# Optimization experiments

Measured on AMD Instinct MI355X. Metric: run time of the kernel, lower is better.

Reference implementation:

```python
import jax, jax.numpy as jnp
import numpy as np

N_HEAD = 16
MASK_VALUE = -10000.0


def setup_inputs() -> dict:
    key = jax.random.key(0)
    k1, k2, k3 = jax.random.split(key, 3)
    B, S, D = 2, 2048, 1024
    x = jax.random.normal(k1, (B, S, D), dtype=jnp.float32)
    W_qkv = jax.random.normal(k2, (D, 3 * D), dtype=jnp.float32) * 0.02
    b_qkv = jnp.zeros((3 * D,), dtype=jnp.float32)
    W_out = jax.random.normal(k3, (D, D), dtype=jnp.float32) * 0.02
    b_out = jnp.zeros((D,), dtype=jnp.float32)
    return {"x": x, "W_qkv": W_qkv, "b_qkv": b_qkv, "W_out": W_out, "b_out": b_out}


def reference(x, W_qkv, b_qkv, W_out, b_out):
    B, S, D = x.shape
    H = N_HEAD
    hd = D // H
    # fused QKV projection
    qkv = x @ W_qkv + b_qkv                      # [B, S, 3D]
    q, k, v = jnp.split(qkv, 3, axis=-1)
    # split heads -> [B, H, S, hd]
    def split_heads(t):
        return t.reshape(B, S, H, hd).transpose(0, 2, 1, 3)
    q, k, v = split_heads(q), split_heads(k), split_heads(v)
    # scaled causal attention with explicit mask-fill (matches ops.attention)
    scale = 1.0 / jnp.sqrt(jnp.asarray(hd, dtype=x.dtype))
    w = jnp.einsum('bhqd,bhkd->bhqk', q, k) * scale   # [B, H, S, S]
    causal = jnp.tril(jnp.ones((S, S), dtype=bool))    # [S, S]
    w = jnp.where(causal, w, jnp.asarray(MASK_VALUE, dtype=w.dtype))
    a = jax.nn.softmax(w, axis=-1)
    o = jnp.einsum('bhqk,bhkd->bhqd', a, v)            # [B, H, S, hd]
    # merge heads -> [B, S, D]
    o = o.transpose(0, 2, 1, 3).reshape(B, S, D)
    out = o @ W_out + b_out
    return out
```

## Files before the change

kernel.cpp:

```cpp
#include <hip/hip_runtime.h>
#include <hip/hip_bf16.h>
#include <stdint.h>

#define BATCH 2
#define SEQ   2048
#define DIM   1024
#define NH    16
#define HD    64
#define MVAL  (-10000.0f)

#if __has_builtin(__builtin_amdgcn_exp2f)
#define EXP2(x) __builtin_amdgcn_exp2f(x)
#define QSCALE  (0.125f * 1.44269504f)
#else
#define EXP2(x) __expf(x)
#define QSCALE  0.125f
#endif

typedef __attribute__((ext_vector_type(8))) short bf16x8;
typedef __attribute__((ext_vector_type(4))) float f32x4;
typedef unsigned short u16;

static __device__ __forceinline__ u16 f2bf(float f) {
  union { float f; uint32_t u; } c; c.f = f;
  uint32_t x = c.u;
  return (u16)((x + 0x7fffu + ((x >> 16) & 1u)) >> 16);
}

static __device__ __forceinline__ uint32_t pk2(float a, float b) {
  __hip_bfloat162 h = __float22bfloat162_rn(make_float2(a, b));
  union { __hip_bfloat162 h; uint32_t u; } c; c.h = h;
  return c.u;
}

static __device__ __forceinline__ int swz128(int row, int chunk) {
  return row * 128 + (((chunk ^ (row & 7)) & 7) << 4);
}

static __device__ __forceinline__ void gload_lds16(const void* g, void* l) {
  __builtin_amdgcn_global_load_lds((const __attribute__((address_space(1))) void*)g,
                                   (__attribute__((address_space(3))) void*)l, 16, 0, 0);
}

__global__ void prep_kernel(const float* __restrict__ x, u16* __restrict__ xb,
                            const float* __restrict__ Wqkv, u16* __restrict__ WqkvT,
                            const float* __restrict__ Wout, u16* __restrict__ WoutT) {
  __shared__ float tile[32][33];
  int blk = blockIdx.x, tid = threadIdx.x;
  if (blk < 4096) {
    int i = blk * 256 + tid;
    float4 v = reinterpret_cast<const float4*>(x)[i];
    reinterpret_cast<uint2*>(xb)[i] = make_uint2(pk2(v.x, v.y), pk2(v.z, v.w));
    return;
  }
  const float* in;
  u16* out;
  int C, t;
  if (blk < 4096 + 3072) { t = blk - 4096; in = Wqkv; out = WqkvT; C = 3072; }
  else                   { t = blk - 7168; in = Wout; out = WoutT; C = 1024; }
  int R = DIM;
  int c0 = (t % (C / 32)) * 32, r0 = (t / (C / 32)) * 32;
  int tx = tid & 31, ty = tid >> 5;
#pragma unroll
  for (int i = 0; i < 32; i += 8)
    tile[ty + i][tx] = in[(size_t)(r0 + ty + i) * C + c0 + tx];
  __syncthreads();
#pragma unroll
  for (int i = 0; i < 32; i += 8)
    out[(size_t)(c0 + ty + i) * R + r0 + tx] = f2bf(tile[tx][ty + i]);
}

template <int EPI>
__global__ __launch_bounds__(256, 2) void gemm_bt_kernel(
    const u16* __restrict__ A, const u16* __restrict__ Bt,
    const float* __restrict__ bias, float* __restrict__ Cout,
    u16* __restrict__ Qo, u16* __restrict__ Ko, u16* __restrict__ Vto,
    int M, int N, int K) {
  __shared__ __align__(16) char lds[32768];
  char* As = lds;
  char* Bs = lds + 16384;
  int tid = threadIdx.x;
  int lane = tid & 63, l15 = lane & 15, l4 = lane >> 4;
  int w = tid >> 6, wr = w >> 1, wc = w & 1;
  int m0 = blockIdx.y * 128, n0 = blockIdx.x * 128;
  int srow = tid >> 3, sch = tid & 7;
  int sc_swz = ((sch ^ (srow & 7)) << 3);

  const u16* Ap = A + (size_t)(m0 + srow) * K + sc_swz;
  const u16* Bp = Bt + (size_t)(n0 + srow) * K + sc_swz;

  f32x4 acc[4][4] = {};

  for (int k0 = 0; k0 < K; k0 += 64) {
    __syncthreads();
#pragma unroll
    for (int i = 0; i < 4; i++) {
      gload_lds16(Ap + (size_t)i * 32 * K + k0, As + i * 4096 + tid * 16);
      gload_lds16(Bp + (size_t)i * 32 * K + k0, Bs + i * 4096 + tid * 16);
    }
    __syncthreads();
#pragma unroll
    for (int ks = 0; ks < 2; ks++) {
      int ch = ks * 4 + l4;
      bf16x8 af[4], bfv[4];
#pragma unroll
      for (int mi = 0; mi < 4; mi++)
        af[mi] = *reinterpret_cast<const bf16x8*>(As + swz128(wr * 64 + mi * 16 + l15, ch));
#pragma unroll
      for (int nj = 0; nj < 4; nj++)
        bfv[nj] = *reinterpret_cast<const bf16x8*>(Bs + swz128(wc * 64 + nj * 16 + l15, ch));
#pragma unroll
      for (int nj = 0; nj < 4; nj++)
#pragma unroll
        for (int mi = 0; mi < 4; mi++)
          acc[nj][mi] = __builtin_amdgcn_mfma_f32_16x16x32_bf16(bfv[nj], af[mi], acc[nj][mi], 0, 0, 0);
    }
  }

#pragma unroll
  for (int nj = 0; nj < 4; nj++) {
    int nb = n0 + wc * 64 + nj * 16 + l4 * 4;
    float4 bv = *reinterpret_cast<const float4*>(bias + nb);
#pragma unroll
    for (int mi = 0; mi < 4; mi++) {
      int m = m0 + wr * 64 + mi * 16 + l15;
      f32x4 a = acc[nj][mi];
      float v0 = a[0] + bv.x, v1 = a[1] + bv.y, v2 = a[2] + bv.z, v3 = a[3] + bv.w;
      if (EPI == 1) {
        *reinterpret_cast<float4*>(Cout + (size_t)m * N + nb) = make_float4(v0, v1, v2, v3);
      } else {
        int b = m >> 11, s = m & 2047;
        int sec = nb >> 10, c = nb & 1023, h = c >> 6, d = c & 63;
        size_t bh = (size_t)(b * NH + h);
        if (sec == 0) {
          *reinterpret_cast<uint2*>(Qo + (bh * SEQ + s) * HD + d) =
              make_uint2(pk2(v0 * QSCALE, v1 * QSCALE), pk2(v2 * QSCALE, v3 * QSCALE));
        } else if (sec == 1) {
          *reinterpret_cast<uint2*>(Ko + (bh * SEQ + s) * HD + d) =
              make_uint2(pk2(v0, v1), pk2(v2, v3));
        } else {
          u16* vt = Vto + (bh * HD + d) * SEQ + s;
          vt[0]       = f2bf(v0);
          vt[SEQ]     = f2bf(v1);
          vt[2 * SEQ] = f2bf(v2);
          vt[3 * SEQ] = f2bf(v3);
        }
      }
    }
  }
}

__global__ __launch_bounds__(256, 2) void attn_kernel(
    const u16* __restrict__ Q, const u16* __restrict__ K,
    const u16* __restrict__ Vt, u16* __restrict__ O) {
  __shared__ __align__(16) char lds[81920];
  int tid = threadIdx.x, lane = tid & 63, w = tid >> 6;
  int l15 = lane & 15, l4 = lane >> 4;
  int sub = w & 1, par = w >> 1;
  int blk = blockIdx.x;
  int bh = (blk & 7) * 4 + ((blk >> 3) & 3);
  int p = blk >> 5;
  const u16* Qh = Q + (size_t)bh * SEQ * HD;
  const u16* Kh = K + (size_t)bh * SEQ * HD;
  const u16* Vh = Vt + (size_t)bh * HD * SEQ;
  char* Pw = lds + 65536 + w * 4096;
  int srow = tid >> 3, sch = tid & 7;
  int b_ = bh >> 4, h_ = bh & 15;

  bf16x8 onesf;
#pragma unroll
  for (int j = 0; j < 8; j++) onesf[j] = (short)0x3F80;

  auto stageKV = [&](int b, int T) {
    const u16* Kt = Kh + (size_t)T * 128 * HD;
    const u16* Vs = Vh + (size_t)T * 128;
    char* Kb = lds + b * 16384;
    char* Vb = lds + 32768 + b * 16384;
#pragma unroll
    for (int i = 0; i < 4; i++) {
      int row = i * 32 + srow;
      int c = (sch ^ (row & 7)) << 3;
      gload_lds16(Kt + (size_t)row * HD + c, Kb + row * 128 + sch * 16);
    }
#pragma unroll
    for (int sv = 0; sv < 2; sv++)
#pragma unroll
      for (int i = 0; i < 2; i++) {
        int d = i * 32 + srow;
        int c = (sch ^ (d & 7)) << 3;
        gload_lds16(Vs + (size_t)d * SEQ + sv * 64 + c, Vb + sv * 8192 + d * 128 + sch * 16);
      }
  };

  int buf = 0;
  stageKV(0, 0);
  __syncthreads();

  for (int pass = 0; pass < 2; pass++) {
    int qt = (pass == 0) ? (31 - p) : p;
    int nT = (qt + 2) >> 1;
    int qb = qt * 64 + sub * 32;

    bf16x8 qf[2][2];
#pragma unroll
    for (int mi = 0; mi < 2; mi++)
#pragma unroll
      for (int ks = 0; ks < 2; ks++)
        qf[mi][ks] = *reinterpret_cast<const bf16x8*>(
            Qh + (size_t)(qb + mi * 16 + l15) * HD + ks * 32 + l4 * 8);

    float mrun[2] = {-1e30f, -1e30f};
    f32x4 oacc[4][2] = {};
    f32x4 acc_l[2] = {};
    bf16x8 pf_c[2][2], vf_c[4][2];
    bool pend = false;

    for (int T = 0; T < nT; T++) {
      int nxt = (T + 1 < nT) ? (T + 1) : (pass == 0 ? 0 : -1);
      if (nxt >= 0) stageKV(buf ^ 1, nxt);

      char* Kw = lds + buf * 16384 + par * 8192;
      char* Vw = lds + 32768 + buf * 16384 + par * 8192;
      int kvb = T * 128 + par * 64;

      __builtin_amdgcn_s_setprio(1);
      if (pend) {
#pragma unroll
        for (int ks = 0; ks < 2; ks++) {
#pragma unroll
          for (int nd = 0; nd < 4; nd++)
#pragma unroll
            for (int mi = 0; mi < 2; mi++)
              oacc[nd][mi] = __builtin_amdgcn_mfma_f32_16x16x32_bf16(
                  vf_c[nd][ks], pf_c[mi][ks], oacc[nd][mi], 0, 0, 0);
#pragma unroll
          for (int mi = 0; mi < 2; mi++)
            acc_l[mi] = __builtin_amdgcn_mfma_f32_16x16x32_bf16(
                onesf, pf_c[mi][ks], acc_l[mi], 0, 0, 0);
        }
      }

      f32x4 s[4][2] = {};
#pragma unroll
      for (int ks = 0; ks < 2; ks++)
#pragma unroll
        for (int nj = 0; nj < 4; nj++) {
          bf16x8 kf = *reinterpret_cast<const bf16x8*>(Kw + swz128(nj * 16 + l15, ks * 4 + l4));
#pragma unroll
          for (int mi = 0; mi < 2; mi++)
            s[nj][mi] = __builtin_amdgcn_mfma_f32_16x16x32_bf16(kf, qf[mi][ks], s[nj][mi], 0, 0, 0);
        }
      __builtin_amdgcn_s_setprio(0);

#pragma unroll
      for (int ks = 0; ks < 2; ks++)
#pragma unroll
        for (int nd = 0; nd < 4; nd++)
          vf_c[nd][ks] = *reinterpret_cast<const bf16x8*>(Vw + swz128(nd * 16 + l15, ks * 4 + l4));

      if (kvb + 63 > qb) {
#pragma unroll
        for (int nj = 0; nj < 4; nj++)
#pragma unroll
          for (int mi = 0; mi < 2; mi++) {
            int qg = qb + mi * 16 + l15;
#pragma unroll
            for (int r = 0; r < 4; r++) {
              int kg = kvb + nj * 16 + l4 * 4 + r;
              if (kg > qg) s[nj][mi][r] = MVAL;
            }
          }
      }

      float mt[2];
#pragma unroll
      for (int mi = 0; mi < 2; mi++) {
        float m = s[0][mi][0];
#pragma unroll
        for (int nj = 0; nj < 4; nj++)
#pragma unroll
          for (int r = 0; r < 4; r++) m = fmaxf(m, s[nj][mi][r]);
        m = fmaxf(m, __shfl_xor(m, 16));
        m = fmaxf(m, __shfl_xor(m, 32));
        mt[mi] = m;
      }

      if (!__all((mt[0] <= mrun[0]) & (mt[1] <= mrun[1]))) {
#pragma unroll
        for (int mi = 0; mi < 2; mi++) {
          float mnew = fmaxf(mrun[mi], mt[mi]);
          float alpha = EXP2(mrun[mi] - mnew);
          mrun[mi] = mnew;
#pragma unroll
          for (int nd = 0; nd < 4; nd++)
#pragma unroll
            for (int r = 0; r < 4; r++) oacc[nd][mi][r] *= alpha;
#pragma unroll
          for (int r = 0; r < 4; r++) acc_l[mi][r] *= alpha;
        }
      }

#pragma unroll
      for (int mi = 0; mi < 2; mi++) {
        int prow = mi * 16 + l15;
#pragma unroll
        for (int nj = 0; nj < 4; nj++) {
          float p0 = EXP2(s[nj][mi][0] - mrun[mi]);
          float p1 = EXP2(s[nj][mi][1] - mrun[mi]);
          float p2 = EXP2(s[nj][mi][2] - mrun[mi]);
          float p3 = EXP2(s[nj][mi][3] - mrun[mi]);
          int chunk = nj * 2 + (l4 >> 1);
          char* dst = Pw + prow * 128 + (((chunk ^ (prow & 7)) & 7) << 4) + (l4 & 1) * 8;
          *reinterpret_cast<uint2*>(dst) = make_uint2(pk2(p0, p1), pk2(p2, p3));
        }
      }

      asm volatile("s_waitcnt lgkmcnt(0)" ::: "memory");
      __builtin_amdgcn_sched_barrier(0);

#pragma unroll
      for (int mi = 0; mi < 2; mi++)
#pragma unroll
        for (int ks = 0; ks < 2; ks++)
          pf_c[mi][ks] = *reinterpret_cast<const bf16x8*>(Pw + swz128(mi * 16 + l15, ks * 4 + l4));
      pend = true;

      __syncthreads();
      buf ^= 1;
    }

    __builtin_amdgcn_s_setprio(1);
#pragma unroll
    for (int ks = 0; ks < 2; ks++) {
#pragma unroll
      for (int nd = 0; nd < 4; nd++)
#pragma unroll
        for (int mi = 0; mi < 2; mi++)
          oacc[nd][mi] = __builtin_amdgcn_mfma_f32_16x16x32_bf16(
              vf_c[nd][ks], pf_c[mi][ks], oacc[nd][mi], 0, 0, 0);
#pragma unroll
      for (int mi = 0; mi < 2; mi++)
        acc_l[mi] = __builtin_amdgcn_mfma_f32_16x16x32_bf16(
            onesf, pf_c[mi][ks], acc_l[mi], 0, 0, 0);
    }
    __builtin_amdgcn_s_setprio(0);

    char* Xo = lds + (buf ^ 1) * 16384;
    float* Xml = (float*)(lds + 65536);
    if (par == 1) {
#pragma unroll
      for (int mi = 0; mi < 2; mi++) {
        int row = sub * 32 + mi * 16 + l15;
        if (l4 == 0) {
          Xml[row * 2] = mrun[mi];
          Xml[row * 2 + 1] = acc_l[mi][0];
        }
#pragma unroll
        for (int nd = 0; nd < 4; nd++)
          *reinterpret_cast<f32x4*>(Xo + row * 256 + (((nd * 4 + l4) ^ (row & 7)) << 4)) =
              oacc[nd][mi];
      }
    }
    __syncthreads();
    if (par == 0) {
#pragma unroll
      for (int mi = 0; mi < 2; mi++) {
        int row = sub * 32 + mi * 16 + l15;
        float mB = Xml[row * 2], lB = Xml[row * 2 + 1];
        float m = fmaxf(mrun[mi], mB);
        float wA = EXP2(mrun[mi] - m), wB = EXP2(mB - m);
        float linv = 1.0f / (acc_l[mi][0] * wA + lB * wB);
        float fA = wA * linv, fB = wB * linv;
        u16* orow = O + ((size_t)b_ * SEQ + qt * 64 + sub * 32 + mi * 16 + l15) * DIM + h_ * HD;
#pragma unroll
        for (int nd = 0; nd < 4; nd++) {
          f32x4 ob = *reinterpret_cast<const f32x4*>(
              Xo + row * 256 + (((nd * 4 + l4) ^ (row & 7)) << 4));
          float o0 = oacc[nd][mi][0] * fA + ob[0] * fB;
          float o1 = oacc[nd][mi][1] * fA + ob[1] * fB;
          float o2 = oacc[nd][mi][2] * fA + ob[2] * fB;
          float o3 = oacc[nd][mi][3] * fA + ob[3] * fB;
          *reinterpret_cast<uint2*>(orow + nd * 16 + l4 * 4) = make_uint2(pk2(o0, o1), pk2(o2, o3));
        }
      }
    }
    __syncthreads();
  }
}

extern "C" void kernel_launch(void* const* d_in, const int* in_sizes, int n_in,
                              void* d_out, int out_size, void* d_ws, size_t ws_size,
                              hipStream_t stream) {
  const float* x     = (const float*)d_in[0];
  const float* W_qkv = (const float*)d_in[1];
  const float* b_qkv = (const float*)d_in[2];
  const float* W_out = (const float*)d_in[3];
  const float* b_out = (const float*)d_in[4];
  float* out = (float*)d_out;
  char* ws = (char*)d_ws;

  u16* xb    = (u16*)(ws);
  u16* WqkvT = (u16*)(ws + 8388608);
  u16* WoutT = (u16*)(ws + 8388608 + 6291456);
  u16* Qb    = (u16*)(ws + 16777216);
  u16* Kb    = (u16*)(ws + 16777216 + 8388608);
  u16* Vtb   = (u16*)(ws + 16777216 + 2 * 8388608);
  u16* Ob    = (u16*)(ws + 16777216 + 3 * 8388608);

  prep_kernel<<<4096 + 3072 + 1024, 256, 0, stream>>>(x, xb, W_qkv, WqkvT, W_out, WoutT);
  gemm_bt_kernel<0><<<dim3(3 * DIM / 128, BATCH * SEQ / 128), 256, 0, stream>>>(
      xb, WqkvT, b_qkv, nullptr, Qb, Kb, Vtb, BATCH * SEQ, 3 * DIM, DIM);
  attn_kernel<<<512, 256, 0, stream>>>(Qb, Kb, Vtb, Ob);
  gemm_bt_kernel<1><<<dim3(DIM / 128, BATCH * SEQ / 128), 256, 0, stream>>>(
      Ob, WoutT, b_out, out, nullptr, nullptr, nullptr, BATCH * SEQ, DIM, DIM);
}
```

Measured before the change: 112.0 us.

## Process both paired query tiles in one KV sweep sharing K/V loads

Instead of two sequential passes over KV for the long (31-p) and short (p) query tiles, the kernel now runs a single KV loop and computes both tiles' scores and outputs from the same staged K/V blocks. This halves K/V global staging for the overlapping range and removes the second pass's pipeline ramp and the extra epilogue barrier. The cost is doubled accumulator register state (two sets of oacc, mrun and acc_l), which raises register pressure against the two-blocks-per-CU launch bound. The previous software pipelining of the PV MFMA into the next iteration is also dropped, and both tiles' P matrices now share the same per-wave LDS scratch in turn.

```diff
diff --git a/kernel.cpp b/kernel.cpp
--- a/kernel.cpp
+++ b/kernel.cpp
@@ -160,6 +160,9 @@
   int blk = blockIdx.x;
   int bh = (blk & 7) * 4 + ((blk >> 3) & 3);
   int p = blk >> 5;
+  int qtA = 31 - p, qtB = p;
+  int nTA = (qtA + 2) >> 1, nTB = (qtB + 2) >> 1;
+  int qbA = qtA * 64 + sub * 32, qbB = qtB * 64 + sub * 32;
   const u16* Qh = Q + (size_t)bh * SEQ * HD;
   const u16* Kh = K + (size_t)bh * SEQ * HD;
   const u16* Vh = Vt + (size_t)bh * HD * SEQ;
@@ -192,86 +195,64 @@
       }
   };
 
+  bf16x8 qfA[2][2], qfB[2][2];
+#pragma unroll
+  for (int mi = 0; mi < 2; mi++)
+#pragma unroll
+    for (int ks = 0; ks < 2; ks++) {
+      qfA[mi][ks] = *reinterpret_cast<const bf16x8*>(
+          Qh + (size_t)(qbA + mi * 16 + l15) * HD + ks * 32 + l4 * 8);
+      qfB[mi][ks] = *reinterpret_cast<const bf16x8*>(
+          Qh + (size_t)(qbB + mi * 16 + l15) * HD + ks * 32 + l4 * 8);
+    }
+
+  float mrunA[2] = {-1e30f, -1e30f}, mrunB[2] = {-1e30f, -1e30f};
+  f32x4 oaccA[4][2] = {}, oaccB[4][2] = {};
+  f32x4 acclA[2] = {}, acclB[2] = {};
+
   int buf = 0;
   stageKV(0, 0);
   __syncthreads();
 
-  for (int pass = 0; pass < 2; pass++) {
-    int qt = (pass == 0) ? (31 - p) : p;
-    int nT = (qt + 2) >> 1;
-    int qb = qt * 64 + sub * 32;
-
-    bf16x8 qf[2][2];
-#pragma unroll
-    for (int mi = 0; mi < 2; mi++)
-#pragma unroll
-      for (int ks = 0; ks < 2; ks++)
-        qf[mi][ks] = *reinterpret_cast<const bf16x8*>(
-            Qh + (size_t)(qb + mi * 16 + l15) * HD + ks * 32 + l4 * 8);
-
-    float mrun[2] = {-1e30f, -1e30f};
-    f32x4 oacc[4][2] = {};
-    f32x4 acc_l[2] = {};
-    bf16x8 pf_c[2][2], vf_c[4][2];
-    bool pend = false;
-
-    for (int T = 0; T < nT; T++) {
-      int nxt = (T + 1 < nT) ? (T + 1) : (pass == 0 ? 0 : -1);
-      if (nxt >= 0) stageKV(buf ^ 1, nxt);
-
-      char* Kw = lds + buf * 16384 + par * 8192;
-      char* Vw = lds + 32768 + buf * 16384 + par * 8192;
-      int kvb = T * 128 + par * 64;
-
-      __builtin_amdgcn_s_setprio(1);
-      if (pend) {
-#pragma unroll
-        for (int ks = 0; ks < 2; ks++) {
-#pragma unroll
-          for (int nd = 0; nd < 4; nd++)
-#pragma unroll
-            for (int mi = 0; mi < 2; mi++)
-              oacc[nd][mi] = __builtin_amdgcn_mfma_f32_16x16x32_bf16(
-                  vf_c[nd][ks], pf_c[mi][ks], oacc[nd][mi], 0, 0, 0);
-#pragma unroll
-          for (int mi = 0; mi < 2; mi++)
-            acc_l[mi] = __builtin_amdgcn_mfma_f32_16x16x32_bf16(
-                onesf, pf_c[mi][ks], acc_l[mi], 0, 0, 0);
-        }
-      }
-
-      f32x4 s[4][2] = {};
-#pragma unroll
-      for (int ks = 0; ks < 2; ks++)
-#pragma unroll
-        for (int nj = 0; nj < 4; nj++) {
-          bf16x8 kf = *reinterpret_cast<const bf16x8*>(Kw + swz128(nj * 16 + l15, ks * 4 + l4));
-#pragma unroll
-          for (int mi = 0; mi < 2; mi++)
-            s[nj][mi] = __builtin_amdgcn_mfma_f32_16x16x32_bf16(kf, qf[mi][ks], s[nj][mi], 0, 0, 0);
-        }
-      __builtin_amdgcn_s_setprio(0);
-
-#pragma unroll
-      for (int ks = 0; ks < 2; ks++)
-#pragma unroll
-        for (int nd = 0; nd < 4; nd++)
-          vf_c[nd][ks] = *reinterpret_cast<const bf16x8*>(Vw + swz128(nd * 16 + l15, ks * 4 + l4));
-
-      if (kvb + 63 > qb) {
-#pragma unroll
-        for (int nj = 0; nj < 4; nj++)
-#pragma unroll
-          for (int mi = 0; mi < 2; mi++) {
-            int qg = qb + mi * 16 + l15;
-#pragma unroll
-            for (int r = 0; r < 4; r++) {
-              int kg = kvb + nj * 16 + l4 * 4 + r;
-              if (kg > qg) s[nj][mi][r] = MVAL;
-            }
+  for (int T = 0; T < nTA; T++) {
+    if (T + 1 < nTA) stageKV(buf ^ 1, T + 1);
+    char* Kw = lds + buf * 16384 + par * 8192;
+    char* Vw = lds + 32768 + buf * 16384 + par * 8192;
+    int kvb = T * 128 + par * 64;
+    bool doB = (T < nTB);
+
+    bf16x8 kf[2][4];
+#pragma unroll
+    for (int ks = 0; ks < 2; ks++)
+#pragma unroll
+      for (int nj = 0; nj < 4; nj++)
+        kf[ks][nj] = *reinterpret_cast<const bf16x8*>(Kw + swz128(nj * 16 + l15, ks * 4 + l4));
+
+    f32x4 s[4][2] = {};
+    __builtin_amdgcn_s_setprio(1);
+#pragma unroll
+    for (int ks = 0; ks < 2; ks++)
+#pragma unroll
+      for (int nj = 0; nj < 4; nj++)
+#pragma unroll
+        for (int mi = 0; mi < 2; mi++)
+          s[nj][mi] = __builtin_amdgcn_mfma_f32_16x16x32_bf16(kf[ks][nj], qfA[mi][ks], s[nj][mi], 0, 0, 0);
+    __builtin_amdgcn_s_setprio(0);
+
+    if (kvb + 63 > qbA) {
+#pragma unroll
+      for (int nj = 0; nj < 4; nj++)
+#pragma unroll
+        for (int mi = 0; mi < 2; mi++) {
+          int qg = qbA + mi * 16 + l15;
+#pragma unroll
+          for (int r = 0; r < 4; r++) {
+            int kg = kvb + nj * 16 + l4 * 4 + r;
+            if (kg > qg) s[nj][mi][r] = MVAL;
           }
-      }
-
+        }
+    }
+    {
       float mt[2];
 #pragma unroll
       for (int mi = 0; mi < 2; mi++) {
@@ -284,107 +265,230 @@
         m = fmaxf(m, __shfl_xor(m, 32));
         mt[mi] = m;
       }
-
-      if (!__all((mt[0] <= mrun[0]) & (mt[1] <= mrun[1]))) {
+      if (!__all((mt[0] <= mrunA[0]) & (mt[1] <= mrunA[1]))) {
 #pragma unroll
         for (int mi = 0; mi < 2; mi++) {
-          float mnew = fmaxf(mrun[mi], mt[mi]);
-          float alpha = EXP2(mrun[mi] - mnew);
-          mrun[mi] = mnew;
+          float mnew = fmaxf(mrunA[mi], mt[mi]);
+          float alpha = EXP2(mrunA[mi] - mnew);
+          mrunA[mi] = mnew;
 #pragma unroll
           for (int nd = 0; nd < 4; nd++)
 #pragma unroll
-            for (int r = 0; r < 4; r++) oacc[nd][mi][r] *= alpha;
-#pragma unroll
-          for (int r = 0; r < 4; r++) acc_l[mi][r] *= alpha;
-        }
-      }
-
+            for (int r = 0; r < 4; r++) oaccA[nd][mi][r] *= alpha;
+#pragma unroll
+          for (int r = 0; r < 4; r++) acclA[mi][r] *= alpha;
+        }
+      }
 #pragma unroll
       for (int mi = 0; mi < 2; mi++) {
         int prow = mi * 16 + l15;
 #pragma unroll
         for (int nj = 0; nj < 4; nj++) {
-          float p0 = EXP2(s[nj][mi][0] - mrun[mi]);
-          float p1 = EXP2(s[nj][mi][1] - mrun[mi]);
-          float p2 = EXP2(s[nj][mi][2] - mrun[mi]);
-          float p3 = EXP2(s[nj][mi][3] - mrun[mi]);
+          float p0 = EXP2(s[nj][mi][0] - mrunA[mi]);
+          float p1 = EXP2(s[nj][mi][1] - mrunA[mi]);
+          float p2 = EXP2(s[nj][mi][2] - mrunA[mi]);
+          float p3 = EXP2(s[nj][mi][3] - mrunA[mi]);
           int chunk = nj * 2 + (l4 >> 1);
           char* dst = Pw + prow * 128 + (((chunk ^ (prow & 7)) & 7) << 4) + (l4 & 1) * 8;
           *reinterpret_cast<uint2*>(dst) = make_uint2(pk2(p0, p1), pk2(p2, p3));
         }
       }
-
+    }
+
+    f32x4 sB[4][2] = {};
+    if (doB) {
+      __builtin_amdgcn_s_setprio(1);
+#pragma unroll
+      for (int ks = 0; ks < 2; ks++)
+#pragma unroll
+        for (int nj = 0; nj < 4; nj++)
+#pragma unroll
+          for (int mi = 0; mi < 2; mi++)
+            sB[nj][mi] = __builtin_amdgcn_mfma_f32_16x16x32_bf16(kf[ks][nj], qfB[mi][ks], sB[nj][mi], 0, 0, 0);
+      __builtin_amdgcn_s_setprio(0);
+    }
+
+    asm volatile("s_waitcnt lgkmcnt(0)" ::: "memory");
+    __builtin_amdgcn_sched_barrier(0);
+    bf16x8 pfA[2][2];
+#pragma unroll
+    for (int mi = 0; mi < 2; mi++)
+#pragma unroll
+      for (int ks = 0; ks < 2; ks++)
+        pfA[mi][ks] = *reinterpret_cast<const bf16x8*>(Pw + swz128(mi * 16 + l15, ks * 4 + l4));
+
+    if (doB) {
+      if (kvb + 63 > qbB) {
+#pragma unroll
+        for (int nj = 0; nj < 4; nj++)
+#pragma unroll
+          for (int mi = 0; mi < 2; mi++) {
+            int qg = qbB + mi * 16 + l15;
+#pragma unroll
+            for (int r = 0; r < 4; r++) {
+              int kg = kvb + nj * 16 + l4 * 4 + r;
+              if (kg > qg) sB[nj][mi][r] = MVAL;
+            }
+          }
+      }
+      float mt[2];
+#pragma unroll
+      for (int mi = 0; mi < 2; mi++) {
+        float m = sB[0][mi][0];
+#pragma unroll
+        for (int nj = 0; nj < 4; nj++)
+#pragma unroll
+          for (int r = 0; r < 4; r++) m = fmaxf(m, sB[nj][mi][r]);
+        m = fmaxf(m, __shfl_xor(m, 16));
+        m = fmaxf(m, __shfl_xor(m, 32));
+        mt[mi] = m;
+      }
+      if (!__all((mt[0] <= mrunB[0]) & (mt[1] <= mrunB[1]))) {
+#pragma unroll
+        for (int mi = 0; mi < 2; mi++) {
+          float mnew = fmaxf(mrunB[mi], mt[mi]);
+          float alpha = EXP2(mrunB[mi] - mnew);
+          mrunB[mi] = mnew;
+#pragma unroll
+          for (int nd = 0; nd < 4; nd++)
+#pragma unroll
+            for (int r = 0; r < 4; r++) oaccB[nd][mi][r] *= alpha;
+#pragma unroll
+          for (int r = 0; r < 4; r++) acclB[mi][r] *= alpha;
+        }
+      }
+#pragma unroll
+      for (int mi = 0; mi < 2; mi++) {
+        int prow = mi * 16 + l15;
+#pragma unroll
+        for (int nj = 0; nj < 4; nj++) {
+          float p0 = EXP2(sB[nj][mi][0] - mrunB[mi]);
+          float p1 = EXP2(sB[nj][mi][1] - mrunB[mi]);
+          float p2 = EXP2(sB[nj][mi][2] - mrunB[mi]);
+          float p3 = EXP2(sB[nj][mi][3] - mrunB[mi]);
+          int chunk = nj * 2 + (l4 >> 1);
+          char* dst = Pw + prow * 128 + (((chunk ^ (prow & 7)) & 7) << 4) + (l4 & 1) * 8;
+          *reinterpret_cast<uint2*>(dst) = make_uint2(pk2(p0, p1), pk2(p2, p3));
+        }
+      }
+    }
+
+    bf16x8 vf[4][2];
+#pragma unroll
+    for (int ks = 0; ks < 2; ks++)
+#pragma unroll
+      for (int nd = 0; nd < 4; nd++)
+        vf[nd][ks] = *reinterpret_cast<const bf16x8*>(Vw + swz128(nd * 16 + l15, ks * 4 + l4));
+
+    __builtin_amdgcn_s_setprio(1);
+#pragma unroll
+    for (int ks = 0; ks < 2; ks++) {
+#pragma unroll
+      for (int nd = 0; nd < 4; nd++)
+#pragma unroll
+        for (int mi = 0; mi < 2; mi++)
+          oaccA[nd][mi] = __builtin_amdgcn_mfma_f32_16x16x32_bf16(
+              vf[nd][ks], pfA[mi][ks], oaccA[nd][mi], 0, 0, 0);
+#pragma unroll
+      for (int mi = 0; mi < 2; mi++)
+        acclA[mi] = __builtin_amdgcn_mfma_f32_16x16x32_bf16(onesf, pfA[mi][ks], acclA[mi], 0, 0, 0);
+    }
+    __builtin_amdgcn_s_setprio(0);
+
+    if (doB) {
       asm volatile("s_waitcnt lgkmcnt(0)" ::: "memory");
       __builtin_amdgcn_sched_barrier(0);
-
+      bf16x8 pfB[2][2];
 #pragma unroll
       for (int mi = 0; mi < 2; mi++)
 #pragma unroll
         for (int ks = 0; ks < 2; ks++)
-          pf_c[mi][ks] = *reinterpret_cast<const bf16x8*>(Pw + swz128(mi * 16 + l15, ks * 4 + l4));
-      pend = true;
-
-      __syncthreads();
-      buf ^= 1;
-    }
-
-    __builtin_amdgcn_s_setprio(1);
-#pragma unroll
-    for (int ks = 0; ks < 2; ks++) {
-#pragma unroll
-      for (int nd = 0; nd < 4; nd++)
+          pfB[mi][ks] = *reinterpret_cast<const bf16x8*>(Pw + swz128(mi * 16 + l15, ks * 4 + l4));
+      __builtin_amdgcn_s_setprio(1);
+#pragma unroll
+      for (int ks = 0; ks < 2; ks++) {
+#pragma unroll
+        for (int nd = 0; nd < 4; nd++)
+#pragma unroll
+          for (int mi = 0; mi < 2; mi++)
+            oaccB[nd][mi] = __builtin_amdgcn_mfma_f32_16x16x32_bf16(
+                vf[nd][ks], pfB[mi][ks], oaccB[nd][mi], 0, 0, 0);
 #pragma unroll
         for (int mi = 0; mi < 2; mi++)
-          oacc[nd][mi] = __builtin_amdgcn_mfma_f32_16x16x32_bf16(
-              vf_c[nd][ks], pf_c[mi][ks], oacc[nd][mi], 0, 0, 0);
-#pragma unroll
-      for (int mi = 0; mi < 2; mi++)
-        acc_l[mi] = __builtin_amdgcn_mfma_f32_16x16x32_bf16(
-            onesf, pf_c[mi][ks], acc_l[mi], 0, 0, 0);
-    }
-    __builtin_amdgcn_s_setprio(0);
-
-    char* Xo = lds + (buf ^ 1) * 16384;
-    float* Xml = (float*)(lds + 65536);
-    if (par == 1) {
-#pragma unroll
-      for (int mi = 0; mi < 2; mi++) {
-        int row = sub * 32 + mi * 16 + l15;
-        if (l4 == 0) {
-          Xml[row * 2] = mrun[mi];
-          Xml[row * 2 + 1] = acc_l[mi][0];
-        }
-#pragma unroll
-        for (int nd = 0; nd < 4; nd++)
-          *reinterpret_cast<f32x4*>(Xo + row * 256 + (((nd * 4 + l4) ^ (row & 7)) << 4)) =
-              oacc[nd][mi];
-      }
-    }
+          acclB[mi] = __builtin_amdgcn_mfma_f32_16x16x32_bf16(onesf, pfB[mi][ks], acclB[mi], 0, 0, 0);
+      }
+      __builtin_amdgcn_s_setprio(0);
+    }
+
     __syncthreads();
-    if (par == 0) {
-#pragma unroll
-      for (int mi = 0; mi < 2; mi++) {
-        int row = sub * 32 + mi * 16 + l15;
-        float mB = Xml[row * 2], lB = Xml[row * 2 + 1];
-        float m = fmaxf(mrun[mi], mB);
-        float wA = EXP2(mrun[mi] - m), wB = EXP2(mB - m);
-        float linv = 1.0f / (acc_l[mi][0] * wA + lB * wB);
+    buf ^= 1;
+  }
+
+  char* XoA = lds + buf * 16384;
+  char* XoB = lds + 32768 + buf * 16384;
+  float* XmlA = (float*)(lds + 65536);
+  float* XmlB = (float*)(lds + 65536 + 8192);
+  if (par == 1) {
+#pragma unroll
+    for (int mi = 0; mi < 2; mi++) {
+      int row = sub * 32 + mi * 16 + l15;
+      if (l4 == 0) {
+        XmlA[row * 2] = mrunA[mi];
+        XmlA[row * 2 + 1] = acclA[mi][0];
+        XmlB[row * 2] = mrunB[mi];
+        XmlB[row * 2 + 1] = acclB[mi][0];
+      }
+#pragma unroll
+      for (int nd = 0; nd < 4; nd++) {
+        *reinterpret_cast<f32x4*>(XoA + row * 256 + (((nd * 4 + l4) ^ (row & 7)) << 4)) =
+            oaccA[nd][mi];
+        *reinterpret_cast<f32x4*>(XoB + row * 256 + (((nd * 4 + l4) ^ (row & 7)) << 4)) =
+            oaccB[nd][mi];
+      }
+    }
+  }
+  __syncthreads();
+  if (par == 0) {
+#pragma unroll
+    for (int mi = 0; mi < 2; mi++) {
+      int row = sub * 32 + mi * 16 + l15;
+      {
+        float mB = XmlA[row * 2], lB = XmlA[row * 2 + 1];
+        float m = fmaxf(mrunA[mi], mB);
+        float wA = EXP2(mrunA[mi] - m), wB = EXP2(mB - m);
+        float linv = 1.0f / (acclA[mi][0] * wA + lB * wB);
         float fA = wA * linv, fB = wB * linv;
-        u16* orow = O + ((size_t)b_ * SEQ + qt * 64 + sub * 32 + mi * 16 + l15) * DIM + h_ * HD;
+        u16* orow = O + ((size_t)b_ * SEQ + qbA + mi * 16 + l15) * DIM + h_ * HD;
 #pragma unroll
         for (int nd = 0; nd < 4; nd++) {
           f32x4 ob = *reinterpret_cast<const f32x4*>(
-              Xo + row * 256 + (((nd * 4 + l4) ^ (row & 7)) << 4));
-          float o0 = oacc[nd][mi][0] * fA + ob[0] * fB;
-          float o1 = oacc[nd][mi][1] * fA + ob[1] * fB;
-          float o2 = oacc[nd][mi][2] * fA + ob[2] * fB;
-          float o3 = oacc[nd][mi][3] * fA + ob[3] * fB;
+              XoA + row * 256 + (((nd * 4 + l4) ^ (row & 7)) << 4));
+          float o0 = oaccA[nd][mi][0] * fA + ob[0] * fB;
+          float o1 = oaccA[nd][mi][1] * fA + ob[1] * fB;
+          float o2 = oaccA[nd][mi][2] * fA + ob[2] * fB;
+          float o3 = oaccA[nd][mi][3] * fA + ob[3] * fB;
           *reinterpret_cast<uint2*>(orow + nd * 16 + l4 * 4) = make_uint2(pk2(o0, o1), pk2(o2, o3));
         }
       }
-    }
-    __syncthreads();
+      {
+        float mB = XmlB[row * 2], lB = XmlB[row * 2 + 1];
+        float m = fmaxf(mrunB[mi], mB);
+        float wA = EXP2(mrunB[mi] - m), wB = EXP2(mB - m);
+        float linv = 1.0f / (acclB[mi][0] * wA + lB * wB);
+        float fA = wA * linv, fB = wB * linv;
+        u16* orow = O + ((size_t)b_ * SEQ + qbB + mi * 16 + l15) * DIM + h_ * HD;
+#pragma unroll
+        for (int nd = 0; nd < 4; nd++) {
+          f32x4 ob = *reinterpret_cast<const f32x4*>(
+              XoB + row * 256 + (((nd * 4 + l4) ^ (row & 7)) << 4));
+          float o0 = oaccB[nd][mi][0] * fA + ob[0] * fB;
+          float o1 = oaccB[nd][mi][1] * fA + ob[1] * fB;
+          float o2 = oaccB[nd][mi][2] * fA + ob[2] * fB;
+          float o3 = oaccB[nd][mi][3] * fA + ob[3] * fB;
+          *reinterpret_cast<uint2*>(orow + nd * 16 + l4 * 4) = make_uint2(pk2(o0, o1), pk2(o2, o3));
+        }
+      }
+    }
   }
 }
 
```

New measurement: 111.0 us. No clear change (-0.9%).

## Single-buffer KV in LDS with register prefetch to raise occupancy to three blocks

Applied to the files above, without the earlier changes.

Replaces double-buffered K/V LDS tiles with a single buffer. K and V fragments are loaded into registers before a barrier, after which the next tile is staged into the freed LDS. LDS per block drops from 80KB to 48KB and launch bounds rise to 3 blocks per CU. This also removes the software-pipelined deferred PV MFMA, so PV now runs in the same iteration. The aim is more resident waves to hide latency, at the cost of an extra barrier per tile, less intra-block overlap and tighter register limits.

```diff
diff --git a/kernel.cpp b/kernel.cpp
--- a/kernel.cpp
+++ b/kernel.cpp
@@ -150,10 +150,10 @@
   }
 }
 
-__global__ __launch_bounds__(256, 2) void attn_kernel(
+__global__ __launch_bounds__(256, 3) void attn_kernel(
     const u16* __restrict__ Q, const u16* __restrict__ K,
     const u16* __restrict__ Vt, u16* __restrict__ O) {
-  __shared__ __align__(16) char lds[81920];
+  __shared__ __align__(16) char lds[49152];
   int tid = threadIdx.x, lane = tid & 63, w = tid >> 6;
   int l15 = lane & 15, l4 = lane >> 4;
   int sub = w & 1, par = w >> 1;
@@ -163,7 +163,7 @@
   const u16* Qh = Q + (size_t)bh * SEQ * HD;
   const u16* Kh = K + (size_t)bh * SEQ * HD;
   const u16* Vh = Vt + (size_t)bh * HD * SEQ;
-  char* Pw = lds + 65536 + w * 4096;
+  char* Pw = lds + 32768 + w * 4096;
   int srow = tid >> 3, sch = tid & 7;
   int b_ = bh >> 4, h_ = bh & 15;
 
@@ -171,11 +171,11 @@
 #pragma unroll
   for (int j = 0; j < 8; j++) onesf[j] = (short)0x3F80;
 
-  auto stageKV = [&](int b, int T) {
+  auto stageKV = [&](int T) {
     const u16* Kt = Kh + (size_t)T * 128 * HD;
     const u16* Vs = Vh + (size_t)T * 128;
-    char* Kb = lds + b * 16384;
-    char* Vb = lds + 32768 + b * 16384;
+    char* Kb = lds;
+    char* Vb = lds + 16384;
 #pragma unroll
     for (int i = 0; i < 4; i++) {
       int row = i * 32 + srow;
@@ -192,10 +192,6 @@
       }
   };
 
-  int buf = 0;
-  stageKV(0, 0);
-  __syncthreads();
-
   for (int pass = 0; pass < 2; pass++) {
     int qt = (pass == 0) ? (31 - p) : p;
     int nT = (qt + 2) >> 1;
@@ -212,51 +208,40 @@
     float mrun[2] = {-1e30f, -1e30f};
     f32x4 oacc[4][2] = {};
     f32x4 acc_l[2] = {};
-    bf16x8 pf_c[2][2], vf_c[4][2];
-    bool pend = false;
+
+    stageKV(0);
+    __syncthreads();
 
     for (int T = 0; T < nT; T++) {
-      int nxt = (T + 1 < nT) ? (T + 1) : (pass == 0 ? 0 : -1);
-      if (nxt >= 0) stageKV(buf ^ 1, nxt);
-
-      char* Kw = lds + buf * 16384 + par * 8192;
-      char* Vw = lds + 32768 + buf * 16384 + par * 8192;
+      char* Kw = lds + par * 8192;
+      char* Vw = lds + 16384 + par * 8192;
       int kvb = T * 128 + par * 64;
 
+      bf16x8 kf[2][4], vf[4][2];
+#pragma unroll
+      for (int ks = 0; ks < 2; ks++)
+#pragma unroll
+        for (int nj = 0; nj < 4; nj++)
+          kf[ks][nj] = *reinterpret_cast<const bf16x8*>(Kw + swz128(nj * 16 + l15, ks * 4 + l4));
+#pragma unroll
+      for (int ks = 0; ks < 2; ks++)
+#pragma unroll
+        for (int nd = 0; nd < 4; nd++)
+          vf[nd][ks] = *reinterpret_cast<const bf16x8*>(Vw + swz128(nd * 16 + l15, ks * 4 + l4));
+
+      __syncthreads();
+      if (T + 1 < nT) stageKV(T + 1);
+
+      f32x4 s[4][2] = {};
       __builtin_amdgcn_s_setprio(1);
-      if (pend) {
-#pragma unroll
-        for (int ks = 0; ks < 2; ks++) {
-#pragma unroll
-          for (int nd = 0; nd < 4; nd++)
-#pragma unroll
-            for (int mi = 0; mi < 2; mi++)
-              oacc[nd][mi] = __builtin_amdgcn_mfma_f32_16x16x32_bf16(
-                  vf_c[nd][ks], pf_c[mi][ks], oacc[nd][mi], 0, 0, 0);
+#pragma unroll
+      for (int ks = 0; ks < 2; ks++)
+#pragma unroll
+        for (int nj = 0; nj < 4; nj++)
 #pragma unroll
           for (int mi = 0; mi < 2; mi++)
-            acc_l[mi] = __builtin_amdgcn_mfma_f32_16x16x32_bf16(
-                onesf, pf_c[mi][ks], acc_l[mi], 0, 0, 0);
-        }
-      }
-
-      f32x4 s[4][2] = {};
-#pragma unroll
-      for (int ks = 0; ks < 2; ks++)
-#pragma unroll
-        for (int nj = 0; nj < 4; nj++) {
-          bf16x8 kf = *reinterpret_cast<const bf16x8*>(Kw + swz128(nj * 16 + l15, ks * 4 + l4));
-#pragma unroll
-          for (int mi = 0; mi < 2; mi++)
-            s[nj][mi] = __builtin_amdgcn_mfma_f32_16x16x32_bf16(kf, qf[mi][ks], s[nj][mi], 0, 0, 0);
-        }
+            s[nj][mi] = __builtin_amdgcn_mfma_f32_16x16x32_bf16(kf[ks][nj], qf[mi][ks], s[nj][mi], 0, 0, 0);
       __builtin_amdgcn_s_setprio(0);
-
-#pragma unroll
-      for (int ks = 0; ks < 2; ks++)
-#pragma unroll
-        for (int nd = 0; nd < 4; nd++)
-          vf_c[nd][ks] = *reinterpret_cast<const bf16x8*>(Vw + swz128(nd * 16 + l15, ks * 4 + l4));
 
       if (kvb + 63 > qb) {
 #pragma unroll
@@ -318,35 +303,33 @@
       asm volatile("s_waitcnt lgkmcnt(0)" ::: "memory");
       __builtin_amdgcn_sched_barrier(0);
 
+      bf16x8 pf[2][2];
 #pragma unroll
       for (int mi = 0; mi < 2; mi++)
 #pragma unroll
         for (int ks = 0; ks < 2; ks++)
-          pf_c[mi][ks] = *reinterpret_cast<const bf16x8*>(Pw + swz128(mi * 16 + l15, ks * 4 + l4));
-      pend = true;
+          pf[mi][ks] = *reinterpret_cast<const bf16x8*>(Pw + swz128(mi * 16 + l15, ks * 4 + l4));
+
+      __builtin_amdgcn_s_setprio(1);
+#pragma unroll
+      for (int ks = 0; ks < 2; ks++) {
+#pragma unroll
+        for (int nd = 0; nd < 4; nd++)
+#pragma unroll
+          for (int mi = 0; mi < 2; mi++)
+            oacc[nd][mi] = __builtin_amdgcn_mfma_f32_16x16x32_bf16(
+                vf[nd][ks], pf[mi][ks], oacc[nd][mi], 0, 0, 0);
+#pragma unroll
+        for (int mi = 0; mi < 2; mi++)
+          acc_l[mi] = __builtin_amdgcn_mfma_f32_16x16x32_bf16(onesf, pf[mi][ks], acc_l[mi], 0, 0, 0);
+      }
+      __builtin_amdgcn_s_setprio(0);
 
       __syncthreads();
-      buf ^= 1;
-    }
-
-    __builtin_amdgcn_s_setprio(1);
-#pragma unroll
-    for (int ks = 0; ks < 2; ks++) {
-#pragma unroll
-      for (int nd = 0; nd < 4; nd++)
-#pragma unroll
-        for (int mi = 0; mi < 2; mi++)
-          oacc[nd][mi] = __builtin_amdgcn_mfma_f32_16x16x32_bf16(
-              vf_c[nd][ks], pf_c[mi][ks], oacc[nd][mi], 0, 0, 0);
-#pragma unroll
-      for (int mi = 0; mi < 2; mi++)
-        acc_l[mi] = __builtin_amdgcn_mfma_f32_16x16x32_bf16(
-            onesf, pf_c[mi][ks], acc_l[mi], 0, 0, 0);
-    }
-    __builtin_amdgcn_s_setprio(0);
-
-    char* Xo = lds + (buf ^ 1) * 16384;
-    float* Xml = (float*)(lds + 65536);
+    }
+
+    char* Xo = lds;
+    float* Xml = (float*)(lds + 16384);
     if (par == 1) {
 #pragma unroll
       for (int mi = 0; mi < 2; mi++) {
```

Result: slower. 155.4 us (+38.8%).
